# Performance work log

Measured on AMD Instinct MI355X. Metric: run time of the kernel, lower is better.

The kernel has to match this reference:

```python
import jax, jax.numpy as jnp
from jax import lax
import numpy as np

KSIZE = 3
NUM_GAB = 16
NUM_IMAP = 16
BATCH = 4096


def gabor_bank(theta, sigma, gamma, lambd, psi, ksize=KSIZE):
    # vectorized version of the original triple Python loop
    offs = jnp.arange(ksize, dtype=theta.dtype) - 1.0  # (x-1), (y-1) in source
    xg, yg = jnp.meshgrid(offs, offs, indexing='ij')   # [K,K]
    c = jnp.cos(theta)[:, None, None]
    s = jnp.sin(theta)[:, None, None]
    xt = xg * c + yg * s        # [F,K,K]
    yt = -xg * s + yg * c
    sx = sigma[:, None, None]
    sy = (sigma / gamma)[:, None, None]
    env = jnp.exp(-0.5 * (xt ** 2 / sx ** 2 + yt ** 2 / sy ** 2))
    car = jnp.cos(2.0 * jnp.pi * xt / lambd[:, None, None] + psi[:, None, None])
    return env * car  # [F,K,K]


def maxpool2(x):
    return lax.reduce_window(x, -jnp.inf, lax.max, (1, 1, 2, 2), (1, 1, 2, 2), 'VALID')


def setup_inputs() -> dict:
    key = jax.random.key(0)
    ks = jax.random.split(key, 12)
    x = jax.random.normal(ks[0], (BATCH, 1, 28, 28), dtype=jnp.float32)
    theta = jax.random.uniform(ks[1], (NUM_GAB,), minval=0.0, maxval=180.0)
    sigma = jax.random.uniform(ks[2], (NUM_GAB,), minval=0.0, maxval=360.0)
    gamma = jax.random.uniform(ks[3], (NUM_GAB,), minval=0.0, maxval=1.0)
    lambd = jax.random.uniform(ks[4], (NUM_GAB,), minval=2.0, maxval=10.0)
    psi = jnp.zeros((NUM_GAB,), dtype=jnp.float32)
    conv2_w = jax.random.normal(ks[5], (64, 32, 3, 3), dtype=jnp.float32) * 0.05
    conv2_b = jnp.zeros((64,), dtype=jnp.float32)
    fc1_w = jax.random.normal(ks[6], (128, 3136), dtype=jnp.float32) * 0.02
    fc1_b = jnp.zeros((128,), dtype=jnp.float32)
    fc2_w = jax.random.normal(ks[7], (10, 128), dtype=jnp.float32) * 0.1
    fc2_b = jnp.zeros((10,), dtype=jnp.float32)
    return dict(x=x, theta=theta, sigma=sigma, gamma=gamma, lambd=lambd, psi=psi,
                conv2_w=conv2_w, conv2_b=conv2_b, fc1_w=fc1_w, fc1_b=fc1_b,
                fc2_w=fc2_w, fc2_b=fc2_b)


def reference(x, theta, sigma, gamma, lambd, psi, conv2_w, conv2_b, fc1_w, fc1_b, fc2_w, fc2_b):
    kern = gabor_bank(theta, sigma, gamma, lambd, psi)          # [16,3,3]
    imaps = jnp.zeros((NUM_IMAP, KSIZE, KSIZE), dtype=x.dtype).at[:, 1, 1].set(1.0)
    w1 = jnp.concatenate([kern, imaps], axis=0)[:, None]         # [32,1,3,3]
    dn = ('NCHW', 'OIHW', 'NCHW')
    out = lax.conv_general_dilated(x, w1, (1, 1), [(1, 1), (1, 1)], dimension_numbers=dn)
    out = maxpool2(jax.nn.relu(out))                             # [B,32,14,14]
    out = lax.conv_general_dilated(out, conv2_w, (1, 1), [(1, 1), (1, 1)], dimension_numbers=dn)
    out = maxpool2(jax.nn.relu(out + conv2_b[None, :, None, None]))  # [B,64,7,7]
    out = out.reshape(out.shape[0], -1)                          # [B,3136]
    out = jax.nn.relu(out @ fc1_w.T + fc1_b)                     # dropout = identity (eval)
    out = out @ fc2_w.T + fc2_b                                  # [B,10]
    return out
```

## Files before the change

kernel.cpp:

```cpp
#include <hip/hip_runtime.h>
#include <hip/hip_bf16.h>

#define BATCH 4096

typedef unsigned short u16;
typedef _Float16 half2v __attribute__((ext_vector_type(2)));
typedef _Float16 half4 __attribute__((ext_vector_type(4)));
typedef _Float16 half8 __attribute__((ext_vector_type(8)));
typedef short bs8 __attribute__((ext_vector_type(8)));
typedef u16 u16x4 __attribute__((ext_vector_type(4)));
typedef float floatx4 __attribute__((ext_vector_type(4)));
typedef float floatx16 __attribute__((ext_vector_type(16)));

__device__ inline u16 f2bf_hw(float f) {
    __hip_bfloat16 b = __float2bfloat16(f);
    return *(u16*)&b;
}

__global__ __launch_bounds__(256) void prep_kernel(
        const float* __restrict__ theta, const float* __restrict__ sigma,
        const float* __restrict__ gamma, const float* __restrict__ lambd,
        const float* __restrict__ psi, const float* __restrict__ conv2_w,
        const float* __restrict__ fc1_w, _Float16* __restrict__ w1h,
        _Float16* __restrict__ w2h, u16* __restrict__ wbf) {
    int id = blockIdx.x * 256 + threadIdx.x;
    if (id < 512) {
        int g = id >> 4, t = id & 15;
        float v = 0.0f;
        if (t < 9) {
            int i = t / 3, j = t % 3;
            float xg = (float)i - 1.0f;
            float yg = (float)j - 1.0f;
            if (g < 16) {
                float th = theta[g];
                float c = cosf(th), s = sinf(th);
                float xt = xg * c + yg * s;
                float yt = -xg * s + yg * c;
                float sx = sigma[g];
                float sy = sx / gamma[g];
                float env = expf(-0.5f *
                                 (xt * xt / (sx * sx) + yt * yt / (sy * sy)));
                float car =
                    cosf(6.28318530717958647692f * xt / lambd[g] + psi[g]);
                v = env * car;
            } else {
                v = (t == 4) ? 1.0f : 0.0f;
            }
        }
        w1h[id] = (_Float16)v;
    } else if (id < 512 + 18432) {
        int t2 = id - 512;
        int tap = t2 / 2048, rem = t2 % 2048;
        int oc = rem / 32, k = rem % 32;
        int ic = (k >> 1) + 16 * (k & 1);
        w2h[t2] = (_Float16)conv2_w[(oc * 32 + ic) * 9 + tap];
    } else {
        int i4 = id - 18944;
        int s = i4 >> 10;
        int q = i4 & 1023;
        int row = q >> 3;
        int k4 = q & 7;
        float4 v = ((const float4*)fc1_w)[row * 784 + s * 8 + k4];
        u16x4 o;
        o[0] = f2bf_hw(v.x);
        o[1] = f2bf_hw(v.y);
        o[2] = f2bf_hw(v.z);
        o[3] = f2bf_hw(v.w);
        ((u16x4*)wbf)[(size_t)s * 1024 + row * 8 + k4] = o;
    }
}

__global__ __launch_bounds__(256) void fused_conv_kernel(
        const float* __restrict__ x, const _Float16* __restrict__ w1h,
        const _Float16* __restrict__ w2h, const float* __restrict__ conv2_b,
        u16* __restrict__ a2) {
    __shared__ _Float16 img16[30][36];
    __shared__ __align__(16) _Float16 a1s[16][16][40];
    __shared__ __align__(16) u16 out2[64 * 49];

    int t = threadIdx.x;
    int n = blockIdx.x;
    int lane = t & 63;
    int w = t >> 6;
    int l16 = lane & 15;
    int quad = lane >> 4;
    int l32 = lane & 31;
    int h = lane >> 5;

    int nt = w & 1;
    int mt0 = w >> 1;
    int oc = nt * 32 + l32;
    half8 bE[9], bO[9];
    const _Float16* bp = w2h + (size_t)oc * 32 + h * 8;
#pragma unroll
    for (int tt = 0; tt < 9; ++tt) {
        bE[tt] = *(const half8*)(bp + tt * 2048);
        bO[tt] = *(const half8*)(bp + tt * 2048 + 16);
    }
    float bias = conv2_b[oc];

    for (int i = t; i < 240; i += 256) {
        int pos = i >> 2, ch = i & 3;
        int r, c;
        if (pos < 16)      { r = 0;        c = pos; }
        else if (pos < 32) { r = 15;       c = pos - 16; }
        else if (pos < 46) { r = pos - 31; c = 0; }
        else               { r = pos - 45; c = 15; }
        *(int4*)&a1s[r][c][ch * 8] = int4{0, 0, 0, 0};
    }
    const float* xim = x + (size_t)n * 784;
    for (int i = t; i < 960; i += 256) {
        int r = i >> 5, c = i & 31;
        bool inter = (r >= 1) & (r <= 28) & (c >= 1) & (c <= 28);
        float v = inter ? xim[(r - 1) * 28 + (c - 1)] : 0.0f;
        img16[r][c] = (_Float16)v;
    }
    __syncthreads();

    half4 b1a = *(const half4*)&w1h[l16 * 16 + quad * 4];
    half4 b1b = *(const half4*)&w1h[(16 + l16) * 16 + quad * 4];
    int t0 = quad * 4;
    int u0 = t0 < 9 ? t0 : 8, u1 = t0 + 1 < 9 ? t0 + 1 : 8;
    int u2 = t0 + 2 < 9 ? t0 + 2 : 8, u3 = t0 + 3 < 9 ? t0 + 3 : 8;
    int off0 = (u0 / 3) * 36 + (u0 % 3);
    int off1 = (u1 / 3) * 36 + (u1 % 3);
    int off2 = (u2 / 3) * 36 + (u2 % 3);
    int off3 = (u3 / 3) * 36 + (u3 % 3);
    int sy = (l16 & 3) >> 1, sx = l16 & 1;

    int pool0 = w * 4 + (l16 >> 2);
    int a14 = pool0 >= 14 ? 1 : 0;
    int b14 = pool0 - 14 * a14;
    int pl0 = w * 4 + quad;
    int pa = pl0 >= 14 ? 1 : 0;
    int pb = pl0 - 14 * pa;

    const _Float16* p0 = &img16[2 * a14 + sy][2 * b14 + sx];
    half4 avc;
    avc[0] = p0[off0];
    avc[1] = p0[off1];
    avc[2] = p0[off2];
    avc[3] = p0[off3];

    for (int mt = w; mt < 49; mt += 4) {
        a14 += 1; b14 += 2;
        if (b14 >= 14) { b14 -= 14; a14 += 1; }
        half4 avn;
        if (mt + 4 < 49) {
            const _Float16* p = &img16[2 * a14 + sy][2 * b14 + sx];
            avn[0] = p[off0];
            avn[1] = p[off1];
            avn[2] = p[off2];
            avn[3] = p[off3];
        }
        floatx4 c0 = {0.f, 0.f, 0.f, 0.f};
        floatx4 c1 = {0.f, 0.f, 0.f, 0.f};
        c0 = __builtin_amdgcn_mfma_f32_16x16x16f16(avc, b1a, c0, 0, 0, 0);
        c1 = __builtin_amdgcn_mfma_f32_16x16x16f16(avc, b1b, c1, 0, 0, 0);
        float m0 = fmaxf(fmaxf(c0[0], c0[1]), fmaxf(c0[2], c0[3]));
        float m1 = fmaxf(fmaxf(c1[0], c1[1]), fmaxf(c1[2], c1[3]));
        half2v pk;
        pk[0] = (_Float16)fmaxf(m0, 0.0f);
        pk[1] = (_Float16)fmaxf(m1, 0.0f);
        *(half2v*)&a1s[1 + pa][1 + pb][2 * l16] = pk;
        pa += 1; pb += 2;
        if (pb >= 14) { pb -= 14; pa += 1; }
        avc = avn;
    }
    __syncthreads();

    for (int mt = mt0; mt < 7; mt += 2) {
        int pool = mt * 8 + (l32 >> 2);
        int sub = l32 & 3;
        int pc = pool < 49 ? pool : 48;
        int y = 2 * (pc / 7) + (sub >> 1);
        int xq = 2 * (pc % 7) + (sub & 1);
        const _Float16* ap = &a1s[y][xq][h * 8];
        floatx16 acc = {};
#pragma unroll
        for (int tt = 0; tt < 9; ++tt) {
            int ao = ((tt / 3) * 16 + (tt % 3)) * 40;
            half8 avE = *(const half8*)(ap + ao);
            half8 avO = *(const half8*)(ap + ao + 16);
            acc = __builtin_amdgcn_mfma_f32_32x32x16_f16(avE, bE[tt], acc,
                                                         0, 0, 0);
            acc = __builtin_amdgcn_mfma_f32_32x32x16_f16(avO, bO[tt], acc,
                                                         0, 0, 0);
        }
#pragma unroll
        for (int rg = 0; rg < 4; ++rg) {
            int pl = mt * 8 + 2 * rg + h;
            if (pl < 49) {
                float v0 = acc[rg * 4 + 0];
                float v1 = acc[rg * 4 + 1];
                float v2 = acc[rg * 4 + 2];
                float v3 = acc[rg * 4 + 3];
                float mx = fmaxf(fmaxf(v0, v1), fmaxf(v2, v3));
                out2[oc * 49 + pl] = f2bf_hw(fmaxf(mx + bias, 0.0f));
            }
        }
    }
    __syncthreads();

    uint2* dst = (uint2*)a2;
    const uint2* src = (const uint2*)&out2[0];
    size_t n8 = (size_t)n * 8;
    for (int i = t; i < 784; i += 256) {
        int s = i >> 3, off = i & 7;
        dst[(size_t)s * 32768 + n8 + off] = src[i];
    }
}

__global__ __launch_bounds__(1024) void fc_kernel(
        const u16* __restrict__ A, const u16* __restrict__ Wbf,
        const float* __restrict__ fc1_b, const float* __restrict__ fc2_w,
        const float* __restrict__ fc2_b, float* __restrict__ out) {
    __shared__ float Hs[8][16][132];
    int tid = threadIdx.x;
    int lane = tid & 63;
    int w = tid >> 6;
    int l16 = lane & 15;
    int quad = lane >> 4;
    int kq = w >> 1;
    int nh = w & 1;
    int m0 = blockIdx.x * 16;

    const u16* abase = A + (size_t)(m0 + l16) * 32 + quad * 8;
    const u16* bbase = Wbf + (size_t)(nh * 64 + l16) * 32 + quad * 8;

    floatx4 ac0 = {0.f, 0.f, 0.f, 0.f};
    floatx4 ac1 = {0.f, 0.f, 0.f, 0.f};
    floatx4 ac2 = {0.f, 0.f, 0.f, 0.f};
    floatx4 ac3 = {0.f, 0.f, 0.f, 0.f};
#pragma unroll 4
    for (int s = kq; s < 98; s += 8) {
        bs8 av = *(const bs8*)(abase + (size_t)s * 131072);
        const u16* bt = bbase + (size_t)s * 4096;
        bs8 bv0 = *(const bs8*)(bt);
        bs8 bv1 = *(const bs8*)(bt + 512);
        bs8 bv2 = *(const bs8*)(bt + 1024);
        bs8 bv3 = *(const bs8*)(bt + 1536);
        ac0 = __builtin_amdgcn_mfma_f32_16x16x32_bf16(av, bv0, ac0, 0, 0, 0);
        ac1 = __builtin_amdgcn_mfma_f32_16x16x32_bf16(av, bv1, ac1, 0, 0, 0);
        ac2 = __builtin_amdgcn_mfma_f32_16x16x32_bf16(av, bv2, ac2, 0, 0, 0);
        ac3 = __builtin_amdgcn_mfma_f32_16x16x32_bf16(av, bv3, ac3, 0, 0, 0);
    }
    int nb = nh * 64 + l16;
#pragma unroll
    for (int r = 0; r < 4; ++r) {
        int mr = quad * 4 + r;
        Hs[kq][mr][nb] = ac0[r];
        Hs[kq][mr][nb + 16] = ac1[r];
        Hs[kq][mr][nb + 32] = ac2[r];
        Hs[kq][mr][nb + 48] = ac3[r];
    }
    __syncthreads();

    for (int i = tid; i < 2048; i += 1024) {
        int m = i >> 7, k = i & 127;
        float s = Hs[0][m][k] + Hs[1][m][k] + Hs[2][m][k] + Hs[3][m][k] +
                  Hs[4][m][k] + Hs[5][m][k] + Hs[6][m][k] + Hs[7][m][k];
        Hs[0][m][k] = s;
    }
    __syncthreads();

    if (tid < 160) {
        int m = tid / 10, j = tid % 10;
        const float* wr = fc2_w + j * 128;
        float acc = fc2_b[j];
#pragma unroll 16
        for (int k = 0; k < 128; ++k)
            acc += fmaxf(Hs[0][m][k] + fc1_b[k], 0.0f) * wr[k];
        out[(size_t)(m0 + m) * 10 + j] = acc;
    }
}

extern "C" void kernel_launch(void* const* d_in, const int* in_sizes, int n_in,
                              void* d_out, int out_size, void* d_ws,
                              size_t ws_size, hipStream_t stream) {
    const float* x       = (const float*)d_in[0];
    const float* theta   = (const float*)d_in[1];
    const float* sigma   = (const float*)d_in[2];
    const float* gamma   = (const float*)d_in[3];
    const float* lambd   = (const float*)d_in[4];
    const float* psi     = (const float*)d_in[5];
    const float* conv2_w = (const float*)d_in[6];
    const float* conv2_b = (const float*)d_in[7];
    const float* fc1_w   = (const float*)d_in[8];
    const float* fc1_b   = (const float*)d_in[9];
    const float* fc2_w   = (const float*)d_in[10];
    const float* fc2_b   = (const float*)d_in[11];
    float* out = (float*)d_out;

    char* ws = (char*)d_ws;
    u16* a2 = (u16*)ws;
    _Float16* w1h = (_Float16*)(ws + 25690112ull);
    _Float16* w2h = (_Float16*)(ws + 25691136ull);
    u16* wbf = (u16*)(ws + 25728000ull);

    prep_kernel<<<466, 256, 0, stream>>>(theta, sigma, gamma, lambd, psi,
                                         conv2_w, fc1_w, w1h, w2h, wbf);
    fused_conv_kernel<<<BATCH, 256, 0, stream>>>(x, w1h, w2h, conv2_b, a2);
    fc_kernel<<<BATCH / 16, 1024, 0, stream>>>(a2, wbf, fc1_b, fc2_w, fc2_b,
                                               out);
}
```

Measured before the change: 149.5 us.

## Defer conv2 weight loads, drop prefetch, transpose conv output layout

The conv2 weight fragment loads move after the conv1 loop, and the conv1 loop's software prefetch of the next input fragment is removed. Together these shorten register live ranges, and the launch bounds now request 4 blocks per SIMD to raise occupancy. Conv output is now stored position-major (pl*64+oc), and the fc1 weight prep permutes its gather to match that new K ordering. The risks are exposed global-load latency for the weights and LDS bank conflicts on the transposed stores.

```diff
diff --git a/kernel.cpp b/kernel.cpp
--- a/kernel.cpp
+++ b/kernel.cpp
@@ -59,18 +59,20 @@
         int s = i4 >> 10;
         int q = i4 & 1023;
         int row = q >> 3;
-        int k4 = q & 7;
-        float4 v = ((const float4*)fc1_w)[row * 784 + s * 8 + k4];
+        int kp = s * 32 + (q & 7) * 4;
+        int pl = kp >> 6;
+        int ocb = kp & 63;
+        const float* src = fc1_w + row * 3136 + ocb * 49 + pl;
         u16x4 o;
-        o[0] = f2bf_hw(v.x);
-        o[1] = f2bf_hw(v.y);
-        o[2] = f2bf_hw(v.z);
-        o[3] = f2bf_hw(v.w);
-        ((u16x4*)wbf)[(size_t)s * 1024 + row * 8 + k4] = o;
-    }
-}
-
-__global__ __launch_bounds__(256) void fused_conv_kernel(
+        o[0] = f2bf_hw(src[0]);
+        o[1] = f2bf_hw(src[49]);
+        o[2] = f2bf_hw(src[98]);
+        o[3] = f2bf_hw(src[147]);
+        ((u16x4*)wbf)[(size_t)s * 1024 + row * 8 + (q & 7)] = o;
+    }
+}
+
+__global__ __launch_bounds__(256, 4) void fused_conv_kernel(
         const float* __restrict__ x, const _Float16* __restrict__ w1h,
         const _Float16* __restrict__ w2h, const float* __restrict__ conv2_b,
         u16* __restrict__ a2) {
@@ -90,14 +92,6 @@
     int nt = w & 1;
     int mt0 = w >> 1;
     int oc = nt * 32 + l32;
-    half8 bE[9], bO[9];
-    const _Float16* bp = w2h + (size_t)oc * 32 + h * 8;
-#pragma unroll
-    for (int tt = 0; tt < 9; ++tt) {
-        bE[tt] = *(const half8*)(bp + tt * 2048);
-        bO[tt] = *(const half8*)(bp + tt * 2048 + 16);
-    }
-    float bias = conv2_b[oc];
 
     for (int i = t; i < 240; i += 256) {
         int pos = i >> 2, ch = i & 3;
@@ -135,38 +129,37 @@
     int pa = pl0 >= 14 ? 1 : 0;
     int pb = pl0 - 14 * pa;
 
-    const _Float16* p0 = &img16[2 * a14 + sy][2 * b14 + sx];
-    half4 avc;
-    avc[0] = p0[off0];
-    avc[1] = p0[off1];
-    avc[2] = p0[off2];
-    avc[3] = p0[off3];
-
     for (int mt = w; mt < 49; mt += 4) {
-        a14 += 1; b14 += 2;
-        if (b14 >= 14) { b14 -= 14; a14 += 1; }
-        half4 avn;
-        if (mt + 4 < 49) {
-            const _Float16* p = &img16[2 * a14 + sy][2 * b14 + sx];
-            avn[0] = p[off0];
-            avn[1] = p[off1];
-            avn[2] = p[off2];
-            avn[3] = p[off3];
-        }
+        const _Float16* p = &img16[2 * a14 + sy][2 * b14 + sx];
+        half4 av;
+        av[0] = p[off0];
+        av[1] = p[off1];
+        av[2] = p[off2];
+        av[3] = p[off3];
         floatx4 c0 = {0.f, 0.f, 0.f, 0.f};
         floatx4 c1 = {0.f, 0.f, 0.f, 0.f};
-        c0 = __builtin_amdgcn_mfma_f32_16x16x16f16(avc, b1a, c0, 0, 0, 0);
-        c1 = __builtin_amdgcn_mfma_f32_16x16x16f16(avc, b1b, c1, 0, 0, 0);
+        c0 = __builtin_amdgcn_mfma_f32_16x16x16f16(av, b1a, c0, 0, 0, 0);
+        c1 = __builtin_amdgcn_mfma_f32_16x16x16f16(av, b1b, c1, 0, 0, 0);
         float m0 = fmaxf(fmaxf(c0[0], c0[1]), fmaxf(c0[2], c0[3]));
         float m1 = fmaxf(fmaxf(c1[0], c1[1]), fmaxf(c1[2], c1[3]));
         half2v pk;
         pk[0] = (_Float16)fmaxf(m0, 0.0f);
         pk[1] = (_Float16)fmaxf(m1, 0.0f);
         *(half2v*)&a1s[1 + pa][1 + pb][2 * l16] = pk;
+        a14 += 1; b14 += 2;
+        if (b14 >= 14) { b14 -= 14; a14 += 1; }
         pa += 1; pb += 2;
         if (pb >= 14) { pb -= 14; pa += 1; }
-        avc = avn;
-    }
+    }
+
+    half8 bE[9], bO[9];
+    const _Float16* bp = w2h + (size_t)oc * 32 + h * 8;
+#pragma unroll
+    for (int tt = 0; tt < 9; ++tt) {
+        bE[tt] = *(const half8*)(bp + tt * 2048);
+        bO[tt] = *(const half8*)(bp + tt * 2048 + 16);
+    }
+    float bias = conv2_b[oc];
     __syncthreads();
 
     for (int mt = mt0; mt < 7; mt += 2) {
@@ -196,7 +189,7 @@
                 float v2 = acc[rg * 4 + 2];
                 float v3 = acc[rg * 4 + 3];
                 float mx = fmaxf(fmaxf(v0, v1), fmaxf(v2, v3));
-                out2[oc * 49 + pl] = f2bf_hw(fmaxf(mx + bias, 0.0f));
+                out2[pl * 64 + oc] = f2bf_hw(fmaxf(mx + bias, 0.0f));
             }
         }
     }
```

Measured after the change: 148.8 us. About the same (-0.5%).
